# Optimization experiments

Hardware: AMD Instinct MI355X
Metric: run time of the kernel (lower is better)

Reference implementation:

```python
import jax, jax.numpy as jnp
import numpy as np

B, T, C, H, W = 32, 64, 2, 32, 32
NK, KS = 16, 6          # n_kernels, kernel_size
ACT = 27                # conv output spatial size (32-6+1)
FEAT = ACT * ACT * NK   # 11664 flattened features
RU = 16                 # rnn_units
AD_RATE_L, REC_RATE_L = 0.1, 0.1   # AdaptiveLayer rates
AD_RATE_R, REC_RATE_R = 0.4, 0.1   # SimpleRNN rates


def setup_inputs() -> dict:
    key = jax.random.key(0)
    ks = jax.random.split(key, 8)
    stdv = 1.0 / np.sqrt(RU)
    return {
        "x": jax.random.normal(ks[0], (B, T, C, H, W), jnp.float32),
        "conv_w": jax.random.normal(ks[1], (NK, C, KS, KS), jnp.float32) * 0.01,
        "conv_b": jnp.full((NK,), 0.01, jnp.float32),
        "w_ih": jax.random.uniform(ks[2], (RU, FEAT), jnp.float32, -stdv, stdv),
        "w_hh": jax.random.uniform(ks[3], (RU, RU), jnp.float32, -stdv, stdv),
        "b_ih": jax.random.uniform(ks[4], (RU,), jnp.float32, -stdv, stdv),
        "b_hh": jax.random.uniform(ks[5], (RU,), jnp.float32, -stdv, stdv),
        "fc_w": jax.random.normal(ks[6], (2, RU), jnp.float32) * 0.01,
        "fc_b": jnp.full((2,), 0.01, jnp.float32),
    }


def reference(x, conv_w, conv_b, w_ih, w_hh, b_ih, b_hh, fc_w, fc_b):
    Bn, Tn = x.shape[:2]
    # per-frame conv: fold frames into batch
    xf = x.reshape(Bn * Tn, C, H, W)
    conv = jax.lax.conv_general_dilated(
        xf, conv_w, window_strides=(1, 1), padding='VALID',
        dimension_numbers=('NCHW', 'OIHW', 'NCHW'))
    conv = conv + conv_b[None, :, None, None]
    out_conv = conv.reshape(Bn, Tn, NK, ACT, ACT)
    out_flat = jax.nn.relu(out_conv.reshape(Bn, Tn, FEAT))

    # AdaptiveLayer: per-frame clamp/decay scan (initial adaptation is zeros)
    def ad_step(adapt, frame):
        out = jnp.maximum(frame - adapt, 0.0)
        adapt = (adapt + AD_RATE_L * out) * (1.0 - REC_RATE_L)
        return adapt, out
    _, adapted = jax.lax.scan(ad_step, jnp.zeros((Bn, FEAT), x.dtype),
                              jnp.swapaxes(out_flat, 0, 1))
    out_adapted = jnp.swapaxes(adapted, 0, 1)  # [B,T,FEAT]

    # SimpleRNN with adaptation state
    def rnn_step(carry, x_t):
        h, adapt = carry
        pre = x_t @ w_ih.T + b_ih + h @ w_hh.T + b_hh
        a = jnp.maximum(pre - adapt, 0.0)
        adapt = (adapt + AD_RATE_R * a) * (1.0 - REC_RATE_R)
        h = jax.nn.relu(a)
        return (h, adapt), h
    h0 = jnp.zeros((Bn, RU), x.dtype)
    _, hs = jax.lax.scan(rnn_step, (h0, h0), jnp.swapaxes(out_adapted, 0, 1))
    out_rnn = jnp.swapaxes(hs, 0, 1)  # [B,T,RU]

    out_fc = out_rnn @ fc_w.T + fc_b  # [B,T,2]
    return (out_fc, out_conv, out_flat, out_rnn)
```

## Files before the change

kernel.cpp:

```cpp
#include <hip/hip_runtime.h>

#define FEAT 11664
#define OFF_FC   0u
#define OFF_CONV 4096u
#define OFF_FLAT 23891968u
#define OFF_RNN  47779840u

static __device__ __forceinline__ unsigned short f2bf(float f) {
    unsigned int u = __float_as_uint(f);
    u += 0x7FFFu + ((u >> 16) & 1u);
    return (unsigned short)(u >> 16);
}

__global__ __launch_bounds__(128) void k_conv(const float* __restrict__ x,
                                              const float* __restrict__ cw,
                                              const float* __restrict__ cb,
                                              float* __restrict__ out)
{
    __shared__ __align__(16) float smem[3456];
    __shared__ float bls[16];
    float* xs  = smem;
    float* wls = smem + 2304;
    float* ot  = smem;
    const int tid = threadIdx.x;
    const int frame = blockIdx.x;

    const float4* xg = (const float4*)(x + (size_t)frame * 2048);
    for (int c0 = tid; c0 < 512; c0 += 128) {
        float4 v = xg[c0];
        int e0 = c0 * 4;
        int ch = e0 >> 10, rem = e0 & 1023, row = rem >> 5, col = rem & 31;
        float* dst = &xs[ch * 1152 + row * 36 + col];
        dst[0] = v.x; dst[1] = v.y; dst[2] = v.z; dst[3] = v.w;
    }
    for (int idx = tid; idx < 1152; idx += 128) {
        int k = idx / 72;
        int rem = idx - k * 72;
        wls[rem * 16 + k] = cw[idx];
    }
    if (tid < 16) bls[tid] = cb[tid];
    __syncthreads();

    const int kg = tid >> 5;
    const int r  = tid & 31;
    float acc[4][27];
    if (r < 27) {
        #pragma unroll
        for (int kk = 0; kk < 4; ++kk)
            #pragma unroll
            for (int c = 0; c < 27; ++c) acc[kk][c] = 0.f;

        for (int ch = 0; ch < 2; ++ch) {
            for (int i = 0; i < 6; ++i) {
                const float* rowp = &xs[ch * 1152 + (r + i) * 36];
                float xr[32];
                #pragma unroll
                for (int m = 0; m < 8; ++m) {
                    float4 v = ((const float4*)rowp)[m];
                    xr[4*m+0] = v.x; xr[4*m+1] = v.y; xr[4*m+2] = v.z; xr[4*m+3] = v.w;
                }
                float4 wj[6];
                #pragma unroll
                for (int j = 0; j < 6; ++j)
                    wj[j] = *(const float4*)&wls[(ch * 36 + i * 6 + j) * 16 + kg * 4];
                #pragma unroll
                for (int j = 0; j < 6; ++j) {
                    #pragma unroll
                    for (int c = 0; c < 27; ++c) {
                        float xv = xr[c + j];
                        acc[0][c] = fmaf(xv, wj[j].x, acc[0][c]);
                        acc[1][c] = fmaf(xv, wj[j].y, acc[1][c]);
                        acc[2][c] = fmaf(xv, wj[j].z, acc[2][c]);
                        acc[3][c] = fmaf(xv, wj[j].w, acc[3][c]);
                    }
                }
            }
        }
    }

    for (int kk = 0; kk < 4; ++kk) {
        __syncthreads();
        if (r < 27) {
            float bv = bls[kg * 4 + kk];
            float* dst = &ot[kg * 729 + r * 27];
            #pragma unroll
            for (int c = 0; c < 27; ++c) dst[c] = acc[kk][c] + bv;
        }
        __syncthreads();
        #pragma unroll
        for (int kg2 = 0; kg2 < 4; ++kg2) {
            const float* src = &ot[kg2 * 729];
            size_t gbase = (size_t)frame * FEAT + (size_t)(kg2 * 4 + kk) * 729;
            for (int e = tid; e < 729; e += 128) {
                float v = src[e];
                out[OFF_CONV + gbase + e] = v;
                out[OFF_FLAT + gbase + e] = v > 0.f ? v : 0.f;
            }
        }
    }
}

typedef short bf16x8 __attribute__((ext_vector_type(8)));
typedef float f32x4  __attribute__((ext_vector_type(4)));

__global__ __launch_bounds__(256) void k_adapt_proj(const float* __restrict__ flat,
                                                    const float* __restrict__ w_ih,
                                                    float* __restrict__ partial)
{
    __shared__ __align__(16) unsigned short A[16 * 744];
    __shared__ __align__(16) unsigned short Bw[16 * 744];
    __shared__ __align__(16) float accscr[4 * 64 * 4];
    const int tid = threadIdx.x;
    const int b  = blockIdx.x >> 4;
    const int fb = blockIdx.x & 15;
    const int fbase = fb * 729;

    for (int n = 0; n < 16; ++n) {
        const float* src = w_ih + (size_t)n * FEAT + fbase;
        for (int f = tid; f < 729; f += 256) Bw[n * 744 + f] = f2bf(src[f]);
    }
    if (tid < 240) {
        int n = tid / 15, c = 729 + (tid % 15);
        A[n * 744 + c]  = 0;
        Bw[n * 744 + c] = 0;
    }
    __syncthreads();

    float ad0 = 0.f, ad1 = 0.f, ad2 = 0.f;
    const int w = tid >> 6, l = tid & 63;
    const int m = l & 15, q = l >> 4;

    for (int tt = 0; tt < 4; ++tt) {
        if (tid < 243) {
            const float* src = flat + (size_t)(b * 64 + tt * 16) * FEAT + fbase + tid * 3;
            float v0[16], v1[16], v2[16];
            #pragma unroll
            for (int tl = 0; tl < 16; ++tl) {
                const float* p = src + (size_t)tl * FEAT;
                v0[tl] = p[0]; v1[tl] = p[1]; v2[tl] = p[2];
            }
            unsigned short* arow = &A[tid * 3];
            #pragma unroll
            for (int tl = 0; tl < 16; ++tl) {
                float o0 = fmaxf(v0[tl] - ad0, 0.f); ad0 = (ad0 + 0.1f * o0) * 0.9f;
                float o1 = fmaxf(v1[tl] - ad1, 0.f); ad1 = (ad1 + 0.1f * o1) * 0.9f;
                float o2 = fmaxf(v2[tl] - ad2, 0.f); ad2 = (ad2 + 0.1f * o2) * 0.9f;
                unsigned short* dst = arow + tl * 744;
                dst[0] = f2bf(o0); dst[1] = f2bf(o1); dst[2] = f2bf(o2);
            }
        }
        __syncthreads();

        f32x4 acc = {0.f, 0.f, 0.f, 0.f};
        for (int s = w; s < 23; s += 4) {
            int k0 = s * 32;
            bf16x8 av = *(const bf16x8*)&A [m * 744 + k0 + q * 8];
            bf16x8 bv = *(const bf16x8*)&Bw[m * 744 + k0 + q * 8];
            acc = __builtin_amdgcn_mfma_f32_16x16x32_bf16(av, bv, acc, 0, 0, 0);
        }
        *(f32x4*)&accscr[(w * 64 + l) * 4] = acc;
        __syncthreads();
        {
            int ll = tid >> 2, rg = tid & 3;
            float s = accscr[(0 * 64 + ll) * 4 + rg] + accscr[(1 * 64 + ll) * 4 + rg]
                    + accscr[(2 * 64 + ll) * 4 + rg] + accscr[(3 * 64 + ll) * 4 + rg];
            int row = ((ll >> 4) * 4) + rg;
            int col = ll & 15;
            partial[(size_t)(((fb * 32 + b) * 64 + tt * 16 + row) * 16) + col] = s;
        }
        __syncthreads();
    }
}

__global__ __launch_bounds__(64) void k_rnn(const float* __restrict__ partial,
                                            const float* __restrict__ w_hh,
                                            const float* __restrict__ b_ih,
                                            const float* __restrict__ b_hh,
                                            const float* __restrict__ fc_w,
                                            const float* __restrict__ fc_b,
                                            float* __restrict__ out)
{
    __shared__ __align__(16) float preL[4096];
    __shared__ float hL[64];
    const int l = threadIdx.x;
    const int bl = l >> 4, u = l & 15;
    const int b = blockIdx.x * 4 + bl;

    const float4* p4 = (const float4*)partial;
    float4* pl4 = (float4*)preL;
    for (int c = l; c < 1024; c += 64) {
        float4 s = {0.f, 0.f, 0.f, 0.f};
        for (int fb = 0; fb < 16; ++fb) {
            float4 v = p4[(size_t)fb * 8192 + blockIdx.x * 1024 + c];
            s.x += v.x; s.y += v.y; s.z += v.z; s.w += v.w;
        }
        pl4[c] = s;
    }

    float wv[16];
    #pragma unroll
    for (int mm = 0; mm < 4; ++mm) {
        float4 t4 = *(const float4*)(w_hh + u * 16 + mm * 4);
        wv[4*mm+0] = t4.x; wv[4*mm+1] = t4.y; wv[4*mm+2] = t4.z; wv[4*mm+3] = t4.w;
    }
    const float bsum = b_ih[u] + b_hh[u];
    float frow[16]; float fcb = 0.f;
    if (u < 2) {
        #pragma unroll
        for (int mm = 0; mm < 4; ++mm) {
            float4 t4 = *(const float4*)(fc_w + u * 16 + mm * 4);
            frow[4*mm+0] = t4.x; frow[4*mm+1] = t4.y; frow[4*mm+2] = t4.z; frow[4*mm+3] = t4.w;
        }
        fcb = fc_b[u];
    }
    hL[l] = 0.f;
    float ad = 0.f;
    __syncthreads();

    for (int t = 0; t < 64; ++t) {
        float hv[16];
        #pragma unroll
        for (int mm = 0; mm < 4; ++mm) {
            float4 h4 = *(const float4*)&hL[bl * 16 + mm * 4];
            hv[4*mm+0] = h4.x; hv[4*mm+1] = h4.y; hv[4*mm+2] = h4.z; hv[4*mm+3] = h4.w;
        }
        if (t > 0 && u < 2) {
            float fcv = fcb;
            #pragma unroll
            for (int v2 = 0; v2 < 16; ++v2) fcv = fmaf(hv[v2], frow[v2], fcv);
            out[OFF_FC + (size_t)(b * 64 + (t - 1)) * 2 + u] = fcv;
        }
        float dot = 0.f;
        #pragma unroll
        for (int v2 = 0; v2 < 16; ++v2) dot = fmaf(hv[v2], wv[v2], dot);
        float v = preL[(bl * 64 + t) * 16 + u] + bsum + dot;
        float a = v - ad; a = a > 0.f ? a : 0.f;
        ad = (ad + 0.4f * a) * 0.9f;
        out[OFF_RNN + (size_t)(b * 64 + t) * 16 + u] = a;
        __syncthreads();
        hL[l] = a;
        __syncthreads();
    }
    {
        float hv[16];
        #pragma unroll
        for (int mm = 0; mm < 4; ++mm) {
            float4 h4 = *(const float4*)&hL[bl * 16 + mm * 4];
            hv[4*mm+0] = h4.x; hv[4*mm+1] = h4.y; hv[4*mm+2] = h4.z; hv[4*mm+3] = h4.w;
        }
        if (u < 2) {
            float fcv = fcb;
            #pragma unroll
            for (int v2 = 0; v2 < 16; ++v2) fcv = fmaf(hv[v2], frow[v2], fcv);
            out[OFF_FC + (size_t)(b * 64 + 63) * 2 + u] = fcv;
        }
    }
}

extern "C" void kernel_launch(void* const* d_in, const int* in_sizes, int n_in,
                              void* d_out, int out_size, void* d_ws, size_t ws_size,
                              hipStream_t stream)
{
    const float* x    = (const float*)d_in[0];
    const float* cw   = (const float*)d_in[1];
    const float* cb   = (const float*)d_in[2];
    const float* w_ih = (const float*)d_in[3];
    const float* w_hh = (const float*)d_in[4];
    const float* b_ih = (const float*)d_in[5];
    const float* b_hh = (const float*)d_in[6];
    const float* fc_w = (const float*)d_in[7];
    const float* fc_b = (const float*)d_in[8];
    float* out = (float*)d_out;
    float* partial = (float*)d_ws;

    k_conv<<<2048, 128, 0, stream>>>(x, cw, cb, out);
    k_adapt_proj<<<512, 256, 0, stream>>>(out + OFF_FLAT, w_ih, partial);
    k_rnn<<<8, 64, 0, stream>>>(partial, w_hh, b_ih, b_hh, fc_w, fc_b, out);
}
```

Before: 345.5 us.

## Stage full conv tile for float4 stores and prefetch next adapt chunk

The conv kernel now stages all 16 output channels in shared memory, 11664 floats, so the conv and relu outputs are written with one contiguous float4 pass instead of four passes separated by barriers. The adapt/projection kernel issues global loads for the next 16-timestep chunk of flat before the MFMA section, so those loads overlap the matrix math, and it hoists the first chunk load above the w_ih conversion. The costs are about 46KB of shared memory per conv block, which can lower occupancy, and more live registers in the adapt kernel.

After: 348.3 us. No clear change (+0.8%).

```diff
diff --git a/kernel.cpp b/kernel.cpp
--- a/kernel.cpp
+++ b/kernel.cpp
@@ -17,7 +17,7 @@
                                               const float* __restrict__ cb,
                                               float* __restrict__ out)
 {
-    __shared__ __align__(16) float smem[3456];
+    __shared__ __align__(16) float smem[11664];
     __shared__ float bls[16];
     float* xs  = smem;
     float* wls = smem + 2304;
@@ -78,25 +78,30 @@
         }
     }
 
-    for (int kk = 0; kk < 4; ++kk) {
-        __syncthreads();
-        if (r < 27) {
+    __syncthreads();
+    if (r < 27) {
+        #pragma unroll
+        for (int kk = 0; kk < 4; ++kk) {
             float bv = bls[kg * 4 + kk];
-            float* dst = &ot[kg * 729 + r * 27];
+            float* dst = &ot[(kg * 4 + kk) * 729 + r * 27];
             #pragma unroll
             for (int c = 0; c < 27; ++c) dst[c] = acc[kk][c] + bv;
         }
-        __syncthreads();
-        #pragma unroll
-        for (int kg2 = 0; kg2 < 4; ++kg2) {
-            const float* src = &ot[kg2 * 729];
-            size_t gbase = (size_t)frame * FEAT + (size_t)(kg2 * 4 + kk) * 729;
-            for (int e = tid; e < 729; e += 128) {
-                float v = src[e];
-                out[OFF_CONV + gbase + e] = v;
-                out[OFF_FLAT + gbase + e] = v > 0.f ? v : 0.f;
-            }
-        }
+    }
+    __syncthreads();
+
+    const float4* src4 = (const float4*)ot;
+    float4* dc = (float4*)(out + OFF_CONV + (size_t)frame * FEAT);
+    float4* df = (float4*)(out + OFF_FLAT + (size_t)frame * FEAT);
+    for (int e = tid; e < 2916; e += 128) {
+        float4 v = src4[e];
+        dc[e] = v;
+        float4 rv;
+        rv.x = v.x > 0.f ? v.x : 0.f;
+        rv.y = v.y > 0.f ? v.y : 0.f;
+        rv.z = v.z > 0.f ? v.z : 0.f;
+        rv.w = v.w > 0.f ? v.w : 0.f;
+        df[e] = rv;
     }
 }
 
@@ -115,6 +120,16 @@
     const int fb = blockIdx.x & 15;
     const int fbase = fb * 729;
 
+    float v0[16], v1[16], v2[16];
+    const float* src0 = flat + (size_t)(b * 64) * FEAT + fbase + tid * 3;
+    if (tid < 243) {
+        #pragma unroll
+        for (int tl = 0; tl < 16; ++tl) {
+            const float* p = src0 + (size_t)tl * FEAT;
+            v0[tl] = p[0]; v1[tl] = p[1]; v2[tl] = p[2];
+        }
+    }
+
     for (int n = 0; n < 16; ++n) {
         const float* src = w_ih + (size_t)n * FEAT + fbase;
         for (int f = tid; f < 729; f += 256) Bw[n * 744 + f] = f2bf(src[f]);
@@ -132,13 +147,6 @@
 
     for (int tt = 0; tt < 4; ++tt) {
         if (tid < 243) {
-            const float* src = flat + (size_t)(b * 64 + tt * 16) * FEAT + fbase + tid * 3;
-            float v0[16], v1[16], v2[16];
-            #pragma unroll
-            for (int tl = 0; tl < 16; ++tl) {
-                const float* p = src + (size_t)tl * FEAT;
-                v0[tl] = p[0]; v1[tl] = p[1]; v2[tl] = p[2];
-            }
             unsigned short* arow = &A[tid * 3];
             #pragma unroll
             for (int tl = 0; tl < 16; ++tl) {
@@ -150,6 +158,15 @@
             }
         }
         __syncthreads();
+
+        if (tt < 3 && tid < 243) {
+            const float* srcn = flat + (size_t)(b * 64 + (tt + 1) * 16) * FEAT + fbase + tid * 3;
+            #pragma unroll
+            for (int tl = 0; tl < 16; ++tl) {
+                const float* p = srcn + (size_t)tl * FEAT;
+                v0[tl] = p[0]; v1[tl] = p[1]; v2[tl] = p[2];
+            }
+        }
 
         f32x4 acc = {0.f, 0.f, 0.f, 0.f};
         for (int s = w; s < 23; s += 4) {
```
